# Kernel optimization log

Hardware: AMD Instinct MI355X
Metric: run time of the kernel (lower is better)

## Reference

```python
import jax, jax.numpy as jnp
import numpy as np

N_VERTS = 1_000_000
N_JOINTS = 55  # SMPL-X: NUM_JOINTS + 1


def setup_inputs() -> dict:
    key = jax.random.key(0)
    k1, k2, k3 = jax.random.split(key, 3)
    points = jax.random.normal(k1, (N_VERTS, 3), dtype=jnp.float32)
    w = jax.random.uniform(k2, (N_VERTS, N_JOINTS), dtype=jnp.float32)
    weights = w / jnp.sum(w, axis=-1, keepdims=True)  # LBS weights sum to 1 per vertex
    SE3 = jax.random.normal(k3, (N_JOINTS, 4, 4), dtype=jnp.float32)
    return {"points": points, "weights": weights, "SE3": SE3}


def reference(points, weights, SE3):
    # RigidTransform.weight: blend per-joint SE(3) matrices with per-vertex weights
    # weights: [N, J], SE3: [J, 4, 4] -> A: [N, 4, 4]
    A = jnp.einsum('nj,jkl->nkl', weights, SE3)
    R = A[:, :3, :3]  # [N, 3, 3]
    T = A[:, :3, 3]   # [N, 3]
    # RigidTransform._transform_points: R @ p + T
    return jnp.einsum('nkl,nl->nk', R, points) + T
```

## Files before the change

kernel.cpp:

```cpp
#include <hip/hip_runtime.h>

#define NJ  55
#define BLK 256

__global__ __launch_bounds__(BLK) void lbs_kernel(
    const float* __restrict__ points,
    const float* __restrict__ weights,
    const float* __restrict__ se3,
    float* __restrict__ out,
    int n_verts)
{
    __shared__ float s_w[BLK * NJ];

    const int tid = threadIdx.x;
    const int block_start = blockIdx.x * BLK;
    const int nv = min(BLK, n_verts - block_start);

    const float* wbase = weights + (size_t)block_start * NJ;
    if (nv == BLK) {
        const float4* src = (const float4*)wbase;
        float4* dst = (float4*)s_w;
        #pragma unroll 4
        for (int i = tid; i < (BLK * NJ) / 4; i += BLK) dst[i] = src[i];
    } else {
        const int total = nv * NJ;
        for (int i = tid; i < total; i += BLK) s_w[i] = wbase[i];
    }
    __syncthreads();

    const int n = block_start + tid;
    if (n >= n_verts) return;

    float A[12];
    #pragma unroll
    for (int e = 0; e < 12; ++e) A[e] = 0.f;

    const float* wr = &s_w[tid * NJ];
    const float4* M = (const float4*)se3;

    #pragma unroll 5
    for (int j = 0; j < NJ; ++j) {
        const float w = wr[j];
        const float4 r0 = M[j * 4 + 0];
        const float4 r1 = M[j * 4 + 1];
        const float4 r2 = M[j * 4 + 2];
        A[0] += w * r0.x; A[1] += w * r0.y; A[2]  += w * r0.z; A[3]  += w * r0.w;
        A[4] += w * r1.x; A[5] += w * r1.y; A[6]  += w * r1.z; A[7]  += w * r1.w;
        A[8] += w * r2.x; A[9] += w * r2.y; A[10] += w * r2.z; A[11] += w * r2.w;
    }

    const float px = points[n * 3 + 0];
    const float py = points[n * 3 + 1];
    const float pz = points[n * 3 + 2];

    out[n * 3 + 0] = A[0] * px + A[1] * py + A[2]  * pz + A[3];
    out[n * 3 + 1] = A[4] * px + A[5] * py + A[6]  * pz + A[7];
    out[n * 3 + 2] = A[8] * px + A[9] * py + A[10] * pz + A[11];
}

extern "C" void kernel_launch(void* const* d_in, const int* in_sizes, int n_in,
                              void* d_out, int out_size, void* d_ws, size_t ws_size,
                              hipStream_t stream) {
    const float* points  = (const float*)d_in[0];
    const float* weights = (const float*)d_in[1];
    const float* se3     = (const float*)d_in[2];
    float* out = (float*)d_out;

    const int n_verts = in_sizes[0] / 3;
    const int grid = (n_verts + BLK - 1) / BLK;
    lbs_kernel<<<grid, BLK, 0, stream>>>(points, weights, se3, out, n_verts);
}
```

Baseline: 318.3 us.

## Read weights directly with aligned float4 loads and stage SE3 in LDS

Drops the per-block LDS staging of the 220 B weight rows. Each thread now reads its own row from global memory with float4 loads, using a per-vertex phase offset so the loads are 16-byte aligned, and handles the three leftover joints with scalar loads. The 55 3x4 SE3 matrices are staged in shared memory, each thread computes two vertices, and launch bounds request higher occupancy. The cost is strided, uncoalesced global access across lanes in exchange for less LDS traffic and more memory-level parallelism; the clamped tail indexing adds some complexity.

After: 464.9 us. +46.1%, slower.

```diff
diff --git a/kernel.cpp b/kernel.cpp
--- a/kernel.cpp
+++ b/kernel.cpp
@@ -2,60 +2,98 @@
 
 #define NJ  55
 #define BLK 256
+#define VPT 2
 
-__global__ __launch_bounds__(BLK) void lbs_kernel(
+__global__ __launch_bounds__(BLK, 6) void lbs_kernel(
     const float* __restrict__ points,
     const float* __restrict__ weights,
     const float* __restrict__ se3,
     float* __restrict__ out,
     int n_verts)
 {
-    __shared__ float s_w[BLK * NJ];
+    __shared__ __align__(16) float sm[NJ * 12];
 
     const int tid = threadIdx.x;
-    const int block_start = blockIdx.x * BLK;
-    const int nv = min(BLK, n_verts - block_start);
-
-    const float* wbase = weights + (size_t)block_start * NJ;
-    if (nv == BLK) {
-        const float4* src = (const float4*)wbase;
-        float4* dst = (float4*)s_w;
-        #pragma unroll 4
-        for (int i = tid; i < (BLK * NJ) / 4; i += BLK) dst[i] = src[i];
-    } else {
-        const int total = nv * NJ;
-        for (int i = tid; i < total; i += BLK) s_w[i] = wbase[i];
+    for (int i = tid; i < NJ * 12; i += BLK) {
+        const int j = i / 12;
+        sm[i] = se3[j * 16 + (i - j * 12)];
     }
     __syncthreads();
 
-    const int n = block_start + tid;
-    if (n >= n_verts) return;
+    const int base = blockIdx.x * (BLK * VPT) + tid;
+    const int p = base & 3;
 
-    float A[12];
+    int nact[VPT];
+    int nc[VPT];
+    const float4* wrow[VPT];
     #pragma unroll
-    for (int e = 0; e < 12; ++e) A[e] = 0.f;
-
-    const float* wr = &s_w[tid * NJ];
-    const float4* M = (const float4*)se3;
-
-    #pragma unroll 5
-    for (int j = 0; j < NJ; ++j) {
-        const float w = wr[j];
-        const float4 r0 = M[j * 4 + 0];
-        const float4 r1 = M[j * 4 + 1];
-        const float4 r2 = M[j * 4 + 2];
-        A[0] += w * r0.x; A[1] += w * r0.y; A[2]  += w * r0.z; A[3]  += w * r0.w;
-        A[4] += w * r1.x; A[5] += w * r1.y; A[6]  += w * r1.z; A[7]  += w * r1.w;
-        A[8] += w * r2.x; A[9] += w * r2.y; A[10] += w * r2.z; A[11] += w * r2.w;
+    for (int v = 0; v < VPT; ++v) {
+        const int n = base + v * BLK;
+        nact[v] = n;
+        nc[v] = (n < n_verts) ? n : (n_verts - 4 + p);
+        wrow[v] = (const float4*)(weights + (size_t)nc[v] * NJ + p);
     }
 
-    const float px = points[n * 3 + 0];
-    const float py = points[n * 3 + 1];
-    const float pz = points[n * 3 + 2];
+    float a[VPT][12];
+    #pragma unroll
+    for (int v = 0; v < VPT; ++v)
+        #pragma unroll
+        for (int e = 0; e < 12; ++e) a[v][e] = 0.f;
 
-    out[n * 3 + 0] = A[0] * px + A[1] * py + A[2]  * pz + A[3];
-    out[n * 3 + 1] = A[4] * px + A[5] * py + A[6]  * pz + A[7];
-    out[n * 3 + 2] = A[8] * px + A[9] * py + A[10] * pz + A[11];
+    #pragma unroll 2
+    for (int k = 0; k < 13; ++k) {
+        float w[VPT][4];
+        #pragma unroll
+        for (int v = 0; v < VPT; ++v) {
+            const float4 t = wrow[v][k];
+            w[v][0] = t.x; w[v][1] = t.y; w[v][2] = t.z; w[v][3] = t.w;
+        }
+        #pragma unroll
+        for (int c = 0; c < 4; ++c) {
+            const float4* sj = (const float4*)&sm[(p + 4 * k + c) * 12];
+            const float4 s0 = sj[0];
+            const float4 s1 = sj[1];
+            const float4 s2 = sj[2];
+            #pragma unroll
+            for (int v = 0; v < VPT; ++v) {
+                const float wc = w[v][c];
+                a[v][0] += wc * s0.x; a[v][1] += wc * s0.y; a[v][2]  += wc * s0.z; a[v][3]  += wc * s0.w;
+                a[v][4] += wc * s1.x; a[v][5] += wc * s1.y; a[v][6]  += wc * s1.z; a[v][7]  += wc * s1.w;
+                a[v][8] += wc * s2.x; a[v][9] += wc * s2.y; a[v][10] += wc * s2.z; a[v][11] += wc * s2.w;
+            }
+        }
+    }
+
+    #pragma unroll
+    for (int i = 0; i < 3; ++i) {
+        int j = p + 52 + i;
+        if (j >= NJ) j -= NJ;
+        const float4* sj = (const float4*)&sm[j * 12];
+        const float4 s0 = sj[0];
+        const float4 s1 = sj[1];
+        const float4 s2 = sj[2];
+        #pragma unroll
+        for (int v = 0; v < VPT; ++v) {
+            const float wc = weights[(size_t)nc[v] * NJ + j];
+            a[v][0] += wc * s0.x; a[v][1] += wc * s0.y; a[v][2]  += wc * s0.z; a[v][3]  += wc * s0.w;
+            a[v][4] += wc * s1.x; a[v][5] += wc * s1.y; a[v][6]  += wc * s1.z; a[v][7]  += wc * s1.w;
+            a[v][8] += wc * s2.x; a[v][9] += wc * s2.y; a[v][10] += wc * s2.z; a[v][11] += wc * s2.w;
+        }
+    }
+
+    #pragma unroll
+    for (int v = 0; v < VPT; ++v) {
+        const float* pp = points + (size_t)nc[v] * 3;
+        const float px = pp[0];
+        const float py = pp[1];
+        const float pz = pp[2];
+        if (nact[v] < n_verts) {
+            float* po = out + (size_t)nact[v] * 3;
+            po[0] = a[v][0] * px + a[v][1] * py + a[v][2]  * pz + a[v][3];
+            po[1] = a[v][4] * px + a[v][5] * py + a[v][6]  * pz + a[v][7];
+            po[2] = a[v][8] * px + a[v][9] * py + a[v][10] * pz + a[v][11];
+        }
+    }
 }
 
 extern "C" void kernel_launch(void* const* d_in, const int* in_sizes, int n_in,
@@ -67,6 +105,7 @@
     float* out = (float*)d_out;
 
     const int n_verts = in_sizes[0] / 3;
-    const int grid = (n_verts + BLK - 1) / BLK;
+    const int per_block = BLK * VPT;
+    const int grid = (n_verts + per_block - 1) / per_block;
     lbs_kernel<<<grid, BLK, 0, stream>>>(points, weights, se3, out, n_verts);
 }
```
